# Performance work log

Measured on AMD Instinct MI355X. Metric: run time of the kernel, lower is better.

## Reference

```python
import jax, jax.numpy as jnp
import numpy as np

N = 50000      # nodes
E = 1_600_000  # edges
D = 512        # input_dim == embedding_dim (see notes: fc_emb output is dead code)
H = 256        # hidden_channels
G = 16         # graphs in the batch


def setup_inputs() -> dict:
    key = jax.random.key(0)
    ks = jax.random.split(key, 16)
    x = jax.random.normal(ks[0], (N, D), dtype=jnp.float32)
    edge_index = jax.random.randint(ks[1], (2, E), 0, N, dtype=jnp.int64)
    batch = jnp.sort(jax.random.randint(ks[2], (N,), 0, G, dtype=jnp.int64))

    def lin(k, fi, fo):
        s = 1.0 / np.sqrt(fi)
        return jax.random.uniform(k, (fi, fo), jnp.float32, -s, s)

    return {
        "x": x,
        "edge_index": edge_index,
        "batch": batch,
        "W1": lin(ks[3], D, H), "b1": jnp.zeros((H,), jnp.float32),
        "W2": lin(ks[4], H, H), "b2": jnp.zeros((H,), jnp.float32),
        "W3": lin(ks[5], H, H), "b3": jnp.zeros((H,), jnp.float32),
        "Wf": lin(ks[6], H, 64), "bf": jnp.zeros((64,), jnp.float32),
        "Wp": lin(ks[7], 64, 1), "bp": jnp.zeros((1,), jnp.float32),
    }


def _gcn_conv(h, src, dst, norm, W, b):
    # GCNConv: out[i] = sum_{j->i} norm_ji * (h[j] @ W) + b  (self-loops included in src/dst)
    m = h @ W                                    # [N, out]  transform first (smaller gather)
    agg = jax.ops.segment_sum(m[src] * norm[:, None], dst, num_segments=N)
    return agg + b


def reference(x, edge_index, batch, W1, b1, W2, b2, W3, b3, Wf, bf, Wp, bp):
    loops = jnp.arange(N, dtype=edge_index.dtype)
    src = jnp.concatenate([edge_index[0], loops])   # [E+N]
    dst = jnp.concatenate([edge_index[1], loops])
    # symmetric normalization D^{-1/2} (A+I) D^{-1/2}; degree over targets incl. self-loops
    deg = jax.ops.segment_sum(jnp.ones_like(dst, jnp.float32), dst, num_segments=N)
    dinv = jnp.where(deg > 0, jax.lax.rsqrt(deg), 0.0)
    norm = dinv[src] * dinv[dst]                    # [E+N]

    h = jax.nn.relu(_gcn_conv(x, src, dst, norm, W1, b1))
    h = jax.nn.relu(_gcn_conv(h, src, dst, norm, W2, b2))
    h = _gcn_conv(h, src, dst, norm, W3, b3)

    # global_mean_pool over graph ids
    counts = jax.ops.segment_sum(jnp.ones((N,), jnp.float32), batch, num_segments=G)
    pooled = jax.ops.segment_sum(h, batch, num_segments=G) / jnp.maximum(counts, 1.0)[:, None]

    # dropout treated as identity (eval-mode determinism for baseline)
    out = pooled @ Wf + bf
    out = out @ Wp + bp
    return jax.nn.sigmoid(out)
```

## Files before the change

### kernel.cpp

```cpp
#include <hip/hip_runtime.h>
#include <hip/hip_bf16.h>

#define NN 50000
#define EE 1600000
#define DD 512
#define HH 256
#define GG 16
#define BK 96
#define NCH 256
#define CHSZ 6250

typedef long fp8x8;
typedef __attribute__((ext_vector_type(4))) float f32x4;
typedef __attribute__((ext_vector_type(2))) float f32x2;

__device__ __forceinline__ float b2f(unsigned short s) {
    union { unsigned int i; float f; } v; v.i = ((unsigned int)s) << 16; return v.f;
}
__device__ __forceinline__ unsigned char f2fp8(float f) {
    return (unsigned char)(__builtin_amdgcn_cvt_pk_fp8_f32(f, f, 0, false) & 0xff);
}
__device__ __forceinline__ unsigned int pk4fp8(float a, float b, float c, float d) {
    unsigned int r = __builtin_amdgcn_cvt_pk_fp8_f32(a, b, 0, false);
    return __builtin_amdgcn_cvt_pk_fp8_f32(c, d, r, true);
}

__global__ __launch_bounds__(256) void k_hist(const int* __restrict__ ei, unsigned int* __restrict__ histg) {
    __shared__ unsigned int hp[12500];
    int b = blockIdx.x, t = threadIdx.x;
    int j = b >> 1, half = b & 1;
    int dlo = half * 25000;
    for (int i = t; i < 12500; i += 256) hp[i] = 0;
    __syncthreads();
    int base = j * CHSZ;
    for (int k = 0; k < 25; ++k) {
        int o = k * 256 + t;
        if (o < CHSZ) {
            int d = ei[EE + base + o];
            unsigned int ld = (unsigned)(d - dlo);
            if (ld < 25000u) atomicAdd(&hp[ld >> 1], (ld & 1) ? 65536u : 1u);
        }
    }
    __syncthreads();
    unsigned int* dst = histg + j * 25000 + half * 12500;
    for (int i = t; i < 12500; i += 256) dst[i] = hp[i];
}

__global__ __launch_bounds__(256) void k_off_cvt(const unsigned int* __restrict__ histg,
                                                 unsigned int* __restrict__ offg,
                                                 int* __restrict__ cnt, float* __restrict__ dinv,
                                                 const float* __restrict__ x, unsigned char* __restrict__ xb,
                                                 const float* __restrict__ W1, const float* __restrict__ W2,
                                                 const float* __restrict__ W3, unsigned char* __restrict__ W1t,
                                                 unsigned char* __restrict__ W2t, unsigned char* __restrict__ W3t) {
    int b = blockIdx.x, t = threadIdx.x;
    if (b < 98) {
        int i = b * 256 + t;
        if (i < 25000) {
            unsigned run0 = 0, run1 = 0;
            #pragma unroll 8
            for (int j = 0; j < NCH; ++j) {
                unsigned h = histg[j * 25000 + i];
                offg[j * 25000 + i] = run0 | (run1 << 16);
                run0 += h & 0xffffu; run1 += h >> 16;
            }
            int d0 = 2 * i, d1 = 2 * i + 1;
            cnt[d0] = (int)run0; cnt[d1] = (int)run1;
            dinv[d0] = rsqrtf((float)run0 + 1.0f);
            dinv[d1] = rsqrtf((float)run1 + 1.0f);
        }
    } else if (b < 6348) {
        size_t i0 = ((size_t)(b - 98) * 256 + t) * 16;
        float4 v0 = *(const float4*)(x + i0);
        float4 v1 = *(const float4*)(x + i0 + 4);
        float4 v2 = *(const float4*)(x + i0 + 8);
        float4 v3 = *(const float4*)(x + i0 + 12);
        uint4 o;
        o.x = pk4fp8(v0.x, v0.y, v0.z, v0.w);
        o.y = pk4fp8(v1.x, v1.y, v1.z, v1.w);
        o.z = pk4fp8(v2.x, v2.y, v2.z, v2.w);
        o.w = pk4fp8(v3.x, v3.y, v3.z, v3.w);
        *(uint4*)(xb + i0) = o;
    } else {
        int u = (b - 6348) * 256 + t;
        if (u < 131072) {
            int k = u >> 8, n = u & 255;
            W1t[(size_t)n * 512 + k] = f2fp8(W1[u]);
        } else if (u < 196608) {
            int q = u - 131072; int k = q >> 8, n = q & 255;
            W2t[(size_t)n * 256 + k] = f2fp8(W2[q]);
        } else {
            int q = u - 196608; int k = q >> 8, n = q & 255;
            W3t[(size_t)n * 256 + k] = f2fp8(W3[q]);
        }
    }
}

__global__ __launch_bounds__(256) void k_place(const int* __restrict__ ei,
                                               const unsigned int* __restrict__ offg,
                                               unsigned short* __restrict__ bucket) {
    __shared__ unsigned int cur[3125];
    int b = blockIdx.x, t = threadIdx.x;
    int x8 = b & 7, j = b >> 3;
    int lo = x8 * CHSZ;
    for (int i = t; i < 3125; i += 256) cur[i] = 0;
    __syncthreads();
    int base = j * CHSZ;
    for (int k = 0; k < 25; ++k) {
        int o = k * 256 + t;
        if (o < CHSZ) {
            int d = ei[EE + base + o];
            unsigned ld = (unsigned)(d - lo);
            if (ld < 6250u) {
                int s = ei[base + o];
                unsigned old = atomicAdd(&cur[ld >> 1], (ld & 1) ? 65536u : 1u);
                unsigned rank = (ld & 1) ? (old >> 16) : (old & 0xffffu);
                unsigned ov = offg[j * 25000 + (d >> 1)];
                unsigned pos = ((d & 1) ? (ov >> 16) : (ov & 0xffffu)) + rank;
                if (pos < BK) bucket[(size_t)d * BK + pos] = (unsigned short)s;
            }
        }
    }
}

__global__ __launch_bounds__(256) void k_gemm_fp8(const unsigned char* __restrict__ A,
                                                  const unsigned char* __restrict__ Bt,
                                                  const float* __restrict__ dinv,
                                                  unsigned char* __restrict__ C, int M, int K) {
    __shared__ unsigned char As[128 * 32];
    __shared__ unsigned char Bs[128 * 32];
    const int tid  = threadIdx.x;
    const int wave = tid >> 6;
    const int lane = tid & 63;
    const int row0 = blockIdx.x * 128;
    const int col0 = blockIdx.y * 128;
    const int wr = wave & 1;
    const int wc = wave >> 1;
    const int l15 = lane & 15;
    const int quad = lane >> 4;

    const int sr = tid >> 1;
    const int sk = (tid & 1) * 16;

    int ar = row0 + sr; if (ar >= M) ar = M - 1;
    const int bc = col0 + sr;

    f32x4 acc[4][4];
    #pragma unroll
    for (int i = 0; i < 4; ++i)
        #pragma unroll
        for (int j = 0; j < 4; ++j)
            acc[i][j] = (f32x4){0.f, 0.f, 0.f, 0.f};

    for (int kb = 0; kb < K; kb += 32) {
        const unsigned char* ga = A + (size_t)ar * K + kb + sk;
        const unsigned char* gb = Bt + (size_t)bc * K + kb + sk;
        __builtin_amdgcn_global_load_lds((const __attribute__((address_space(1))) void*)ga,
            (__attribute__((address_space(3))) void*)&As[wave * 1024], 16, 0, 0);
        __builtin_amdgcn_global_load_lds((const __attribute__((address_space(1))) void*)gb,
            (__attribute__((address_space(3))) void*)&Bs[wave * 1024], 16, 0, 0);
        __syncthreads();

        fp8x8 af[4], bfr[4];
        #pragma unroll
        for (int mi = 0; mi < 4; ++mi)
            af[mi] = *(const fp8x8*)&As[(wr * 64 + mi * 16 + l15) * 32 + quad * 8];
        #pragma unroll
        for (int ni = 0; ni < 4; ++ni)
            bfr[ni] = *(const fp8x8*)&Bs[(wc * 64 + ni * 16 + l15) * 32 + quad * 8];
        #pragma unroll
        for (int mi = 0; mi < 4; ++mi)
            #pragma unroll
            for (int ni = 0; ni < 4; ++ni)
                acc[mi][ni] = __builtin_amdgcn_mfma_f32_16x16x32_fp8_fp8(af[mi], bfr[ni], acc[mi][ni], 0, 0, 0);
        __syncthreads();
    }

    #pragma unroll
    for (int mi = 0; mi < 4; ++mi) {
        #pragma unroll
        for (int r = 0; r < 4; ++r) {
            int grow = row0 + wr * 64 + mi * 16 + quad * 4 + r;
            if (grow < M) {
                float ds = dinv[grow];
                #pragma unroll
                for (int ni = 0; ni < 4; ++ni) {
                    int gcol = col0 + wc * 64 + ni * 16 + l15;
                    C[(size_t)grow * 256 + gcol] = f2fp8(ds * acc[mi][ni][r]);
                }
            }
        }
    }
}

__global__ __launch_bounds__(256) void k_agg(const unsigned int* __restrict__ m,
                                             const float* __restrict__ bias,
                                             const float* __restrict__ dinv, const int* __restrict__ cnt,
                                             const unsigned short* __restrict__ bucket,
                                             unsigned int* __restrict__ outb,
                                             int do_relu) {
    int lane = threadIdx.x & 63;
    int node = blockIdx.x * 4 + (threadIdx.x >> 6);
    if (node >= NN) return;
    const unsigned int* mrow = m + lane;
    unsigned int v = mrow[(size_t)node * 64];
    f32x2 lo = __builtin_amdgcn_cvt_pk_f32_fp8(v, false);
    f32x2 hi = __builtin_amdgcn_cvt_pk_f32_fp8(v, true);
    float4 acc = make_float4(lo.x, lo.y, hi.x, hi.y);
    int n = cnt[node]; if (n > BK) n = BK;
    const unsigned short* cs = bucket + (size_t)node * BK;
    int p = 0;
    for (; p + 8 <= n; p += 8) {
        int s0 = cs[p], s1 = cs[p + 1], s2 = cs[p + 2], s3 = cs[p + 3];
        int s4 = cs[p + 4], s5 = cs[p + 5], s6 = cs[p + 6], s7 = cs[p + 7];
        unsigned int u0 = mrow[(size_t)s0 * 64];
        unsigned int u1 = mrow[(size_t)s1 * 64];
        unsigned int u2 = mrow[(size_t)s2 * 64];
        unsigned int u3 = mrow[(size_t)s3 * 64];
        unsigned int u4 = mrow[(size_t)s4 * 64];
        unsigned int u5 = mrow[(size_t)s5 * 64];
        unsigned int u6 = mrow[(size_t)s6 * 64];
        unsigned int u7 = mrow[(size_t)s7 * 64];
        f32x2 a0 = __builtin_amdgcn_cvt_pk_f32_fp8(u0, false), b0 = __builtin_amdgcn_cvt_pk_f32_fp8(u0, true);
        f32x2 a1 = __builtin_amdgcn_cvt_pk_f32_fp8(u1, false), b1 = __builtin_amdgcn_cvt_pk_f32_fp8(u1, true);
        f32x2 a2 = __builtin_amdgcn_cvt_pk_f32_fp8(u2, false), b2 = __builtin_amdgcn_cvt_pk_f32_fp8(u2, true);
        f32x2 a3 = __builtin_amdgcn_cvt_pk_f32_fp8(u3, false), b3 = __builtin_amdgcn_cvt_pk_f32_fp8(u3, true);
        f32x2 a4 = __builtin_amdgcn_cvt_pk_f32_fp8(u4, false), b4 = __builtin_amdgcn_cvt_pk_f32_fp8(u4, true);
        f32x2 a5 = __builtin_amdgcn_cvt_pk_f32_fp8(u5, false), b5 = __builtin_amdgcn_cvt_pk_f32_fp8(u5, true);
        f32x2 a6 = __builtin_amdgcn_cvt_pk_f32_fp8(u6, false), b6 = __builtin_amdgcn_cvt_pk_f32_fp8(u6, true);
        f32x2 a7 = __builtin_amdgcn_cvt_pk_f32_fp8(u7, false), b7 = __builtin_amdgcn_cvt_pk_f32_fp8(u7, true);
        acc.x += ((a0.x + a1.x) + (a2.x + a3.x)) + ((a4.x + a5.x) + (a6.x + a7.x));
        acc.y += ((a0.y + a1.y) + (a2.y + a3.y)) + ((a4.y + a5.y) + (a6.y + a7.y));
        acc.z += ((b0.x + b1.x) + (b2.x + b3.x)) + ((b4.x + b5.x) + (b6.x + b7.x));
        acc.w += ((b0.y + b1.y) + (b2.y + b3.y)) + ((b4.y + b5.y) + (b6.y + b7.y));
    }
    for (; p < n; ++p) {
        int s = cs[p];
        unsigned int u = mrow[(size_t)s * 64];
        f32x2 a = __builtin_amdgcn_cvt_pk_f32_fp8(u, false);
        f32x2 b = __builtin_amdgcn_cvt_pk_f32_fp8(u, true);
        acc.x += a.x; acc.y += a.y; acc.z += b.x; acc.w += b.y;
    }
    float di = dinv[node];
    const float4 bb = *(const float4*)(bias + lane * 4);
    acc.x = acc.x * di + bb.x; acc.y = acc.y * di + bb.y;
    acc.z = acc.z * di + bb.z; acc.w = acc.w * di + bb.w;
    if (do_relu) {
        acc.x = fmaxf(acc.x, 0.f); acc.y = fmaxf(acc.y, 0.f);
        acc.z = fmaxf(acc.z, 0.f); acc.w = fmaxf(acc.w, 0.f);
    }
    outb[(size_t)node * 64 + lane] = pk4fp8(acc.x, acc.y, acc.z, acc.w);
}

__global__ __launch_bounds__(256) void k_pool(const unsigned int* __restrict__ h,
                                              const int* __restrict__ batch,
                                              float* __restrict__ pooled, float* __restrict__ cnts) {
    __shared__ float pl[GG * 256];
    __shared__ float cl[GG];
    int t = threadIdx.x;
    for (int i = t; i < GG * 256; i += 256) pl[i] = 0.f;
    if (t < GG) cl[t] = 0.f;
    __syncthreads();
    int sub = t >> 6;
    int fd = t & 63;
    int chunk = (NN + gridDim.x - 1) / gridDim.x;
    int i0 = blockIdx.x * chunk;
    int i1 = i0 + chunk; if (i1 > NN) i1 = NN;
    int gcur = -1;
    float a0 = 0.f, a1 = 0.f, a2 = 0.f, a3 = 0.f, cr = 0.f;
    for (int i = i0 + sub; i < i1; i += 4) {
        int g = batch[i];
        if (g != gcur) {
            if (gcur >= 0) {
                atomicAdd(&pl[gcur * 256 + fd * 4 + 0], a0);
                atomicAdd(&pl[gcur * 256 + fd * 4 + 1], a1);
                atomicAdd(&pl[gcur * 256 + fd * 4 + 2], a2);
                atomicAdd(&pl[gcur * 256 + fd * 4 + 3], a3);
                if (fd == 0) atomicAdd(&cl[gcur], cr);
            }
            gcur = g; a0 = a1 = a2 = a3 = 0.f; cr = 0.f;
        }
        unsigned int u = h[(size_t)i * 64 + fd];
        f32x2 lo = __builtin_amdgcn_cvt_pk_f32_fp8(u, false);
        f32x2 hi = __builtin_amdgcn_cvt_pk_f32_fp8(u, true);
        a0 += lo.x; a1 += lo.y; a2 += hi.x; a3 += hi.y;
        cr += 1.f;
    }
    if (gcur >= 0) {
        atomicAdd(&pl[gcur * 256 + fd * 4 + 0], a0);
        atomicAdd(&pl[gcur * 256 + fd * 4 + 1], a1);
        atomicAdd(&pl[gcur * 256 + fd * 4 + 2], a2);
        atomicAdd(&pl[gcur * 256 + fd * 4 + 3], a3);
        if (fd == 0) atomicAdd(&cl[gcur], cr);
    }
    __syncthreads();
    for (int i = t; i < GG * 256; i += 256)
        if (pl[i] != 0.f) atomicAdd(&pooled[i], pl[i]);
    if (t < GG && cl[t] != 0.f) atomicAdd(&cnts[t], cl[t]);
}

__global__ __launch_bounds__(1024) void k_head(const float* __restrict__ pooled, const float* __restrict__ cnts,
                                               const float* __restrict__ Wf, const float* __restrict__ bf,
                                               const float* __restrict__ Wp, const float* __restrict__ bp,
                                               float* __restrict__ out) {
    __shared__ float z[GG][64];
    int t = threadIdx.x;
    int g = t >> 6, j = t & 63;
    float inv = 1.f / fmaxf(cnts[g], 1.f);
    float acc = 0.f;
    for (int k = 0; k < 256; ++k) acc += pooled[g * 256 + k] * Wf[k * 64 + j];
    z[g][j] = acc * inv + bf[j];
    __syncthreads();
    if (t < GG) {
        float o = 0.f;
        for (int j2 = 0; j2 < 64; ++j2) o += z[t][j2] * Wp[j2];
        o += bp[0];
        out[t] = 1.f / (1.f + expf(-o));
    }
}

extern "C" void kernel_launch(void* const* d_in, const int* in_sizes, int n_in,
                              void* d_out, int out_size, void* d_ws, size_t ws_size,
                              hipStream_t stream) {
    const float* x   = (const float*)d_in[0];
    const int*   ei  = (const int*)d_in[1];
    const int*   bat = (const int*)d_in[2];
    const float* W1  = (const float*)d_in[3];
    const float* b1  = (const float*)d_in[4];
    const float* W2  = (const float*)d_in[5];
    const float* b2  = (const float*)d_in[6];
    const float* W3  = (const float*)d_in[7];
    const float* b3  = (const float*)d_in[8];
    const float* Wf  = (const float*)d_in[9];
    const float* bf  = (const float*)d_in[10];
    const float* Wp  = (const float*)d_in[11];
    const float* bp  = (const float*)d_in[12];
    float* out = (float*)d_out;

    char* w = (char*)d_ws;
    unsigned char* xb  = (unsigned char*)w;  w += (size_t)NN * DD;
    unsigned char* mb  = (unsigned char*)w;  w += (size_t)NN * HH;
    unsigned char* hb  = (unsigned char*)w;  w += (size_t)NCH * 25000 * 4;
    unsigned char* hb2 = (unsigned char*)w;  w += (size_t)NCH * 25000 * 4;
    unsigned char* W1t = (unsigned char*)w;  w += (size_t)DD * HH;
    unsigned char* W2t = (unsigned char*)w;  w += (size_t)HH * HH;
    unsigned char* W3t = (unsigned char*)w;  w += (size_t)HH * HH;
    float* dinv   = (float*)w;               w += (size_t)NN * 4;
    int*   cnt    = (int*)w;                 w += (size_t)NN * 4;
    unsigned short* bucket = (unsigned short*)w; w += (size_t)NN * BK * 2;
    float* pooled = (float*)w;               w += (size_t)GG * HH * 4;
    float* cnts   = (float*)w;               w += (size_t)GG * 4;

    unsigned int* histg = (unsigned int*)hb;
    unsigned int* offg  = (unsigned int*)hb2;

    hipMemsetAsync(pooled, 0, (size_t)(GG * HH + GG) * 4, stream);

    k_hist<<<512, 256, 0, stream>>>(ei, histg);
    k_off_cvt<<<7372, 256, 0, stream>>>(histg, offg, cnt, dinv, x, xb, W1, W2, W3, W1t, W2t, W3t);
    k_place<<<2048, 256, 0, stream>>>(ei, offg, bucket);

    dim3 gg((NN + 127) / 128, 2);
    k_gemm_fp8<<<gg, 256, 0, stream>>>(xb, W1t, dinv, mb, NN, DD);
    k_agg<<<(NN + 3) / 4, 256, 0, stream>>>((const unsigned int*)mb, b1, dinv, cnt, bucket,
                                            (unsigned int*)hb, 1);
    k_gemm_fp8<<<gg, 256, 0, stream>>>(hb, W2t, dinv, mb, NN, HH);
    k_agg<<<(NN + 3) / 4, 256, 0, stream>>>((const unsigned int*)mb, b2, dinv, cnt, bucket,
                                            (unsigned int*)hb2, 1);
    k_gemm_fp8<<<gg, 256, 0, stream>>>(hb2, W3t, dinv, mb, NN, HH);
    k_agg<<<(NN + 3) / 4, 256, 0, stream>>>((const unsigned int*)mb, b3, dinv, cnt, bucket,
                                            (unsigned int*)hb, 0);

    k_pool<<<256, 256, 0, stream>>>((const unsigned int*)hb, bat, pooled, cnts);
    k_head<<<1, 1024, 0, stream>>>(pooled, cnts, Wf, bf, Wp, bp, out);
}
```

Baseline: 552.4 us.

## Split histogram into quarters, fuse with conversions, parallelize offset scan

Each histogram block now covers a quarter of the destination range using a smaller shared array, and the histogram work is merged with the fp8 conversion of x and the weights in one launch. The column-wise prefix scan moves into its own kernel where 8 warps each handle 32 chunks, combining partial sums through shared memory, instead of one thread walking all 256 chunks serially with only 98 blocks. The aim is more parallelism on the serial scan and better occupancy for the histogram, at the cost of reading the edge list twice as often during histogramming and an extra kernel launch.

```diff
diff --git a/kernel.cpp b/kernel.cpp
--- a/kernel.cpp
+++ b/kernel.cpp
@@ -25,52 +25,33 @@
     return __builtin_amdgcn_cvt_pk_fp8_f32(c, d, r, true);
 }
 
-__global__ __launch_bounds__(256) void k_hist(const int* __restrict__ ei, unsigned int* __restrict__ histg) {
-    __shared__ unsigned int hp[12500];
+__global__ __launch_bounds__(256) void k_hist_cvt(const int* __restrict__ ei,
+                                                  unsigned int* __restrict__ histg,
+                                                  const float* __restrict__ x, unsigned char* __restrict__ xb,
+                                                  const float* __restrict__ W1, const float* __restrict__ W2,
+                                                  const float* __restrict__ W3, unsigned char* __restrict__ W1t,
+                                                  unsigned char* __restrict__ W2t, unsigned char* __restrict__ W3t) {
+    __shared__ unsigned int hp[6250];
     int b = blockIdx.x, t = threadIdx.x;
-    int j = b >> 1, half = b & 1;
-    int dlo = half * 25000;
-    for (int i = t; i < 12500; i += 256) hp[i] = 0;
-    __syncthreads();
-    int base = j * CHSZ;
-    for (int k = 0; k < 25; ++k) {
-        int o = k * 256 + t;
-        if (o < CHSZ) {
-            int d = ei[EE + base + o];
-            unsigned int ld = (unsigned)(d - dlo);
-            if (ld < 25000u) atomicAdd(&hp[ld >> 1], (ld & 1) ? 65536u : 1u);
-        }
-    }
-    __syncthreads();
-    unsigned int* dst = histg + j * 25000 + half * 12500;
-    for (int i = t; i < 12500; i += 256) dst[i] = hp[i];
-}
-
-__global__ __launch_bounds__(256) void k_off_cvt(const unsigned int* __restrict__ histg,
-                                                 unsigned int* __restrict__ offg,
-                                                 int* __restrict__ cnt, float* __restrict__ dinv,
-                                                 const float* __restrict__ x, unsigned char* __restrict__ xb,
-                                                 const float* __restrict__ W1, const float* __restrict__ W2,
-                                                 const float* __restrict__ W3, unsigned char* __restrict__ W1t,
-                                                 unsigned char* __restrict__ W2t, unsigned char* __restrict__ W3t) {
-    int b = blockIdx.x, t = threadIdx.x;
-    if (b < 98) {
-        int i = b * 256 + t;
-        if (i < 25000) {
-            unsigned run0 = 0, run1 = 0;
-            #pragma unroll 8
-            for (int j = 0; j < NCH; ++j) {
-                unsigned h = histg[j * 25000 + i];
-                offg[j * 25000 + i] = run0 | (run1 << 16);
-                run0 += h & 0xffffu; run1 += h >> 16;
+    if (b < 1024) {
+        int j = b >> 2, q = b & 3;
+        int dlo = q * 12500;
+        for (int i = t; i < 6250; i += 256) hp[i] = 0;
+        __syncthreads();
+        int base = j * CHSZ;
+        for (int k = 0; k < 25; ++k) {
+            int o = k * 256 + t;
+            if (o < CHSZ) {
+                int d = ei[EE + base + o];
+                unsigned int ld = (unsigned)(d - dlo);
+                if (ld < 12500u) atomicAdd(&hp[ld >> 1], (ld & 1) ? 65536u : 1u);
             }
-            int d0 = 2 * i, d1 = 2 * i + 1;
-            cnt[d0] = (int)run0; cnt[d1] = (int)run1;
-            dinv[d0] = rsqrtf((float)run0 + 1.0f);
-            dinv[d1] = rsqrtf((float)run1 + 1.0f);
-        }
-    } else if (b < 6348) {
-        size_t i0 = ((size_t)(b - 98) * 256 + t) * 16;
+        }
+        __syncthreads();
+        unsigned int* dst = histg + j * 25000 + q * 6250;
+        for (int i = t; i < 6250; i += 256) dst[i] = hp[i];
+    } else if (b < 7274) {
+        size_t i0 = ((size_t)(b - 1024) * 256 + t) * 16;
         float4 v0 = *(const float4*)(x + i0);
         float4 v1 = *(const float4*)(x + i0 + 4);
         float4 v2 = *(const float4*)(x + i0 + 8);
@@ -82,7 +63,7 @@
         o.w = pk4fp8(v3.x, v3.y, v3.z, v3.w);
         *(uint4*)(xb + i0) = o;
     } else {
-        int u = (b - 6348) * 256 + t;
+        int u = (b - 7274) * 256 + t;
         if (u < 131072) {
             int k = u >> 8, n = u & 255;
             W1t[(size_t)n * 512 + k] = f2fp8(W1[u]);
@@ -92,6 +73,48 @@
         } else {
             int q = u - 196608; int k = q >> 8, n = q & 255;
             W3t[(size_t)n * 256 + k] = f2fp8(W3[q]);
+        }
+    }
+}
+
+__global__ __launch_bounds__(256) void k_scan(const unsigned int* __restrict__ histg,
+                                              unsigned int* __restrict__ offg,
+                                              int* __restrict__ cnt, float* __restrict__ dinv) {
+    __shared__ unsigned int part[8][32];
+    int t = threadIdx.x;
+    int il = t & 31, g = t >> 5;
+    int i = blockIdx.x * 32 + il;
+    bool ok = (i < 25000);
+    unsigned int hv[32];
+    unsigned int p0 = 0, p1 = 0;
+    if (ok) {
+        const unsigned int* hp = histg + (size_t)(g * 32) * 25000 + i;
+        #pragma unroll
+        for (int jj = 0; jj < 32; ++jj) hv[jj] = hp[(size_t)jj * 25000];
+        #pragma unroll
+        for (int jj = 0; jj < 32; ++jj) { p0 += hv[jj] & 0xffffu; p1 += hv[jj] >> 16; }
+    }
+    part[g][il] = p0 | (p1 << 16);
+    __syncthreads();
+    unsigned int b0 = 0, b1 = 0;
+    #pragma unroll
+    for (int g2 = 0; g2 < 7; ++g2) {
+        if (g2 < g) { unsigned int p = part[g2][il]; b0 += p & 0xffffu; b1 += p >> 16; }
+    }
+    if (ok && g == 7) {
+        unsigned int tot0 = b0 + p0, tot1 = b1 + p1;
+        cnt[2 * i]     = (int)tot0;
+        cnt[2 * i + 1] = (int)tot1;
+        dinv[2 * i]     = rsqrtf((float)tot0 + 1.0f);
+        dinv[2 * i + 1] = rsqrtf((float)tot1 + 1.0f);
+    }
+    if (ok) {
+        unsigned int run0 = b0, run1 = b1;
+        unsigned int* op = offg + (size_t)(g * 32) * 25000 + i;
+        #pragma unroll
+        for (int jj = 0; jj < 32; ++jj) {
+            op[(size_t)jj * 25000] = run0 | (run1 << 16);
+            run0 += hv[jj] & 0xffffu; run1 += hv[jj] >> 16;
         }
     }
 }
@@ -356,8 +379,8 @@
 
     hipMemsetAsync(pooled, 0, (size_t)(GG * HH + GG) * 4, stream);
 
-    k_hist<<<512, 256, 0, stream>>>(ei, histg);
-    k_off_cvt<<<7372, 256, 0, stream>>>(histg, offg, cnt, dinv, x, xb, W1, W2, W3, W1t, W2t, W3t);
+    k_hist_cvt<<<8298, 256, 0, stream>>>(ei, histg, x, xb, W1, W2, W3, W1t, W2t, W3t);
+    k_scan<<<782, 256, 0, stream>>>(histg, offg, cnt, dinv);
     k_place<<<2048, 256, 0, stream>>>(ei, offg, bucket);
 
     dim3 gg((NN + 127) / 128, 2);
```

Result: no change. 546.2 us (-1.1%).
